# Performance work log

Hardware: AMD Instinct MI355X
Metric: run time of the kernel (lower is better)

The kernel has to match this reference:

```python
import jax, jax.numpy as jnp
import numpy as np

THRESHOLDS = (0.25, 0.375, 0.5, 0.625)
NUM_CLASSES = 5
SMOOTH = 1e-5  # dice smoothing constant


def setup_inputs() -> dict:
    key = jax.random.key(0)
    k1, k2 = jax.random.split(key)
    # [N, T, C, H, W]; input has 5 class channels, target 1 intensity channel
    inp = jax.random.uniform(k1, (4, 10, 5, 384, 384), dtype=jnp.float32)
    tgt = jax.random.uniform(k2, (4, 10, 1, 384, 384), dtype=jnp.float32)
    weight = jnp.array([1.0, 1.0, 2.0, 5.0, 10.0], dtype=jnp.float32)
    return {"input": inp, "target": tgt, "weight": weight}


def reference(input, target, weight):
    # permute to [N, C, T, H, W]
    x = jnp.transpose(input, (0, 2, 1, 3, 4))   # [N,5,T,H,W]
    t = jnp.transpose(target, (0, 2, 1, 3, 4))  # [N,1,T,H,W]
    # threshold binning: class index = number of thresholds <= target value
    cls = jnp.zeros(t.shape, dtype=jnp.int32)
    for thr in THRESHOLDS:
        cls = cls + (t >= thr).astype(jnp.int32)
    # one-hot scatter along class dim -> [N,5,T,H,W]
    class_ids = jnp.arange(NUM_CLASSES, dtype=jnp.int32).reshape(1, NUM_CLASSES, 1, 1, 1)
    onehot = (cls == class_ids).astype(x.dtype)
    # per-class dice over all remaining dims
    axes = (0, 2, 3, 4)
    inter = jnp.sum(x * onehot, axis=axes)                      # [5]
    denom = jnp.sum(x, axis=axes) + jnp.sum(onehot, axis=axes)  # [5]
    dice_loss = 1.0 - (2.0 * inter + SMOOTH) / (denom + SMOOTH)  # [5]
    return jnp.sum(weight * dice_loss)
```

## Files before the change

kernel.cpp:

```cpp
#include <hip/hip_runtime.h>

#define HW      147456
#define GPS     36864
#define NC      5
#define NT      40
#define BX      36
#define ITERS   4
#define NPB     1440
#define SMOOTH  1e-5f


__global__ __launch_bounds__(256) void dice_main(const float* __restrict__ inp,
                                                 const float* __restrict__ tgt,
                                                 float* __restrict__ ws) {
    const int c  = blockIdx.y;
    const int nt = blockIdx.z;
    const int g0 = blockIdx.x * 1024 + threadIdx.x;

    const float4* __restrict__ tb =
        reinterpret_cast<const float4*>(tgt + (size_t)nt * (size_t)HW);
    const float4* __restrict__ ib =
        reinterpret_cast<const float4*>(inp + ((size_t)nt * NC + c) * (size_t)HW);

    float4 t4[ITERS], x4[ITERS];
    #pragma unroll
    for (int it = 0; it < ITERS; ++it) {
        const int g = g0 + it * 256;
        t4[it] = tb[g];
        x4[it] = ib[g];
    }

    float sumx = 0.f, inter = 0.f, cntf = 0.f;
    #pragma unroll
    for (int it = 0; it < ITERS; ++it) {
        const float4 t = t4[it];
        const float4 x = x4[it];
        sumx += (x.x + x.y) + (x.z + x.w);

        const int b0 = (t.x >= 0.25f) + (t.x >= 0.375f) + (t.x >= 0.5f) + (t.x >= 0.625f);
        const int b1 = (t.y >= 0.25f) + (t.y >= 0.375f) + (t.y >= 0.5f) + (t.y >= 0.625f);
        const int b2 = (t.z >= 0.25f) + (t.z >= 0.375f) + (t.z >= 0.5f) + (t.z >= 0.625f);
        const int b3 = (t.w >= 0.25f) + (t.w >= 0.375f) + (t.w >= 0.5f) + (t.w >= 0.625f);

        float iv = 0.f, cv = 0.f;
        if (b0 == c) { iv += x.x; cv += 1.f; }
        if (b1 == c) { iv += x.y; cv += 1.f; }
        if (b2 == c) { iv += x.z; cv += 1.f; }
        if (b3 == c) { iv += x.w; cv += 1.f; }
        inter += iv;
        cntf  += cv;
    }

    float v[3] = {sumx, inter, cntf};
    #pragma unroll
    for (int j = 0; j < 3; ++j) {
        #pragma unroll
        for (int off = 32; off > 0; off >>= 1)
            v[j] += __shfl_down(v[j], off, 64);
    }

    __shared__ float part[4][3];
    const int lane = threadIdx.x & 63;
    const int wv   = threadIdx.x >> 6;
    if (lane == 0) {
        #pragma unroll
        for (int j = 0; j < 3; ++j) part[wv][j] = v[j];
    }
    __syncthreads();
    if (threadIdx.x < 3) {
        const float s = part[0][threadIdx.x] + part[1][threadIdx.x] +
                        part[2][threadIdx.x] + part[3][threadIdx.x];
        ws[((size_t)c * 3 + threadIdx.x) * NPB + (nt * BX + blockIdx.x)] = s;
    }
}

__global__ __launch_bounds__(960) void dice_final(const float* __restrict__ ws,
                                                  const float* __restrict__ w,
                                                  float* __restrict__ out) {
    __shared__ float red[15];
    const int s    = threadIdx.x >> 6;
    const int lane = threadIdx.x & 63;

    float acc = 0.f;
    for (int b = lane; b < NPB; b += 64)
        acc += ws[s * NPB + b];

    #pragma unroll
    for (int off = 32; off > 0; off >>= 1)
        acc += __shfl_down(acc, off, 64);

    if (lane == 0) red[s] = acc;
    __syncthreads();

    if (threadIdx.x == 0) {
        float loss = 0.f;
        #pragma unroll
        for (int c = 0; c < NC; ++c) {
            const float sumx  = red[c * 3 + 0];
            const float inter = red[c * 3 + 1];
            const float cnt   = red[c * 3 + 2];
            const float denom = sumx + cnt;
            loss += w[c] * (1.f - (2.f * inter + SMOOTH) / (denom + SMOOTH));
        }
        out[0] = loss;
    }
}

extern "C" void kernel_launch(void* const* d_in, const int* in_sizes, int n_in,
                              void* d_out, int out_size, void* d_ws, size_t ws_size,
                              hipStream_t stream) {
    const float* inp = (const float*)d_in[0];
    const float* tgt = (const float*)d_in[1];
    const float* wgt = (const float*)d_in[2];
    float* out = (float*)d_out;
    float* ws  = (float*)d_ws;

    dice_main<<<dim3(BX, NC, NT), 256, 0, stream>>>(inp, tgt, ws);
    dice_final<<<1, 960, 0, stream>>>(ws, wgt, out);
}
```

Before: 191.3 us.

## Remap blocks so same-chunk class blocks share an XCD and double per-thread work

Switches to a 1D grid and decodes block index so that the five class blocks reading the same target chunk land on the same XCD (round-robin by blockIdx mod 8), improving L2 reuse of the target tensor. It also halves the number of x-blocks and doubles loads per thread (ITERS 8), issuing all target loads before input loads. This trades fewer, heavier blocks and more registers for better cache locality and memory-level parallelism.

```diff
diff --git a/kernel.cpp b/kernel.cpp
--- a/kernel.cpp
+++ b/kernel.cpp
@@ -4,38 +4,43 @@
 #define GPS     36864
 #define NC      5
 #define NT      40
-#define BX      36
-#define ITERS   4
-#define NPB     1440
+#define BX      18
+#define NK      (BX * NT)
+#define ITERS   8
+#define NBLOCKS (NK * NC)
 #define SMOOTH  1e-5f
 
 
 __global__ __launch_bounds__(256) void dice_main(const float* __restrict__ inp,
                                                  const float* __restrict__ tgt,
                                                  float* __restrict__ ws) {
-    const int c  = blockIdx.y;
-    const int nt = blockIdx.z;
-    const int g0 = blockIdx.x * 1024 + threadIdx.x;
+    const int f   = blockIdx.x;
+    const int xcd = f & 7;
+    const int r   = f >> 3;
+    const int c   = r % 5;
+    const int k   = (r / 5) * 8 + xcd;
+    const int nt  = k / BX;
+    const int x   = k - nt * BX;
 
     const float4* __restrict__ tb =
         reinterpret_cast<const float4*>(tgt + (size_t)nt * (size_t)HW);
     const float4* __restrict__ ib =
         reinterpret_cast<const float4*>(inp + ((size_t)nt * NC + c) * (size_t)HW);
 
+    const int g0 = x * (256 * ITERS) + threadIdx.x;
+
     float4 t4[ITERS], x4[ITERS];
     #pragma unroll
-    for (int it = 0; it < ITERS; ++it) {
-        const int g = g0 + it * 256;
-        t4[it] = tb[g];
-        x4[it] = ib[g];
-    }
+    for (int it = 0; it < ITERS; ++it) t4[it] = tb[g0 + it * 256];
+    #pragma unroll
+    for (int it = 0; it < ITERS; ++it) x4[it] = ib[g0 + it * 256];
 
     float sumx = 0.f, inter = 0.f, cntf = 0.f;
     #pragma unroll
     for (int it = 0; it < ITERS; ++it) {
         const float4 t = t4[it];
-        const float4 x = x4[it];
-        sumx += (x.x + x.y) + (x.z + x.w);
+        const float4 x4v = x4[it];
+        sumx += (x4v.x + x4v.y) + (x4v.z + x4v.w);
 
         const int b0 = (t.x >= 0.25f) + (t.x >= 0.375f) + (t.x >= 0.5f) + (t.x >= 0.625f);
         const int b1 = (t.y >= 0.25f) + (t.y >= 0.375f) + (t.y >= 0.5f) + (t.y >= 0.625f);
@@ -43,10 +48,10 @@
         const int b3 = (t.w >= 0.25f) + (t.w >= 0.375f) + (t.w >= 0.5f) + (t.w >= 0.625f);
 
         float iv = 0.f, cv = 0.f;
-        if (b0 == c) { iv += x.x; cv += 1.f; }
-        if (b1 == c) { iv += x.y; cv += 1.f; }
-        if (b2 == c) { iv += x.z; cv += 1.f; }
-        if (b3 == c) { iv += x.w; cv += 1.f; }
+        if (b0 == c) { iv += x4v.x; cv += 1.f; }
+        if (b1 == c) { iv += x4v.y; cv += 1.f; }
+        if (b2 == c) { iv += x4v.z; cv += 1.f; }
+        if (b3 == c) { iv += x4v.w; cv += 1.f; }
         inter += iv;
         cntf  += cv;
     }
@@ -70,7 +75,7 @@
     if (threadIdx.x < 3) {
         const float s = part[0][threadIdx.x] + part[1][threadIdx.x] +
                         part[2][threadIdx.x] + part[3][threadIdx.x];
-        ws[((size_t)c * 3 + threadIdx.x) * NPB + (nt * BX + blockIdx.x)] = s;
+        ws[((size_t)c * 3 + threadIdx.x) * NK + k] = s;
     }
 }
 
@@ -82,8 +87,8 @@
     const int lane = threadIdx.x & 63;
 
     float acc = 0.f;
-    for (int b = lane; b < NPB; b += 64)
-        acc += ws[s * NPB + b];
+    for (int b = lane; b < NK; b += 64)
+        acc += ws[s * NK + b];
 
     #pragma unroll
     for (int off = 32; off > 0; off >>= 1)
@@ -115,6 +120,6 @@
     float* out = (float*)d_out;
     float* ws  = (float*)d_ws;
 
-    dice_main<<<dim3(BX, NC, NT), 256, 0, stream>>>(inp, tgt, ws);
+    dice_main<<<NBLOCKS, 256, 0, stream>>>(inp, tgt, ws);
     dice_final<<<1, 960, 0, stream>>>(ws, wgt, out);
 }
```

Result: no change. 191.3 us (-0.0%).
